# Optimization experiments

Hardware: AMD Instinct MI355X
Metric: run time of the kernel (lower is better)

The kernel has to match this reference:

```python
import jax, jax.numpy as jnp
import numpy as np
import math

N_NODES = 16000
N_EDGES = 256000
F = 64            # channels per irrep (hidden = 64x0e + 64x1o)
Z = 4             # num chemical elements
R = 8             # radial embedding dim
AVG_NN = 16.0
LS = (0, 1, 2)
OFF = {0: 0, 1: 1, 2: 4}
DIM = {0: 1, 1: 3, 2: 5}
SH_DIM = 9
# tensor-product paths (l1, l2, l3), parity-allowed (l1+l2+l3 even), l3 <= 2
PATHS_I0 = ((0, 0, 0), (0, 1, 1), (0, 2, 2))
PATHS_I1 = ((0, 0, 0), (0, 1, 1), (0, 2, 2), (1, 0, 1), (1, 1, 0), (1, 1, 2), (1, 2, 1))
PATHS_P = ((0, 0, 0), (0, 1, 1), (0, 2, 2), (1, 0, 1), (1, 1, 0), (1, 1, 2), (1, 2, 1), (2, 0, 2), (2, 1, 1), (2, 2, 0), (2, 2, 2))


def _cg_complex(l1, l2, l3):
    f = math.factorial
    C = np.zeros((2 * l1 + 1, 2 * l2 + 1, 2 * l3 + 1))
    pre0 = math.sqrt((2 * l3 + 1) * f(l3 + l1 - l2) * f(l3 - l1 + l2) * f(l1 + l2 - l3) / f(l1 + l2 + l3 + 1))
    for m1 in range(-l1, l1 + 1):
        for m2 in range(-l2, l2 + 1):
            m3 = m1 + m2
            if abs(m3) > l3:
                continue
            pre = pre0 * math.sqrt(f(l3 + m3) * f(l3 - m3) * f(l1 - m1) * f(l1 + m1) * f(l2 - m2) * f(l2 + m2))
            s = 0.0
            for k in range(0, l1 + l2 - l3 + 1):
                d = (k, l1 + l2 - l3 - k, l1 - m1 - k, l2 + m2 - k, l3 - l2 + m1 + k, l3 - l1 - m2 + k)
                if min(d) < 0:
                    continue
                den = 1.0
                for x in d:
                    den *= f(x)
                s += (-1) ** k / den
            C[m1 + l1, m2 + l2, m3 + l3] = pre * s
    return C


def _c2r(l):
    # complex -> real spherical-harmonic change of basis (rows: real m, cols: complex m)
    A = np.zeros((2 * l + 1, 2 * l + 1), dtype=complex)
    A[l, l] = 1.0
    s = 1.0 / math.sqrt(2.0)
    for m in range(1, l + 1):
        A[l + m, l + m] = (-1) ** m * s
        A[l + m, l - m] = s
        A[l - m, l + m] = -1j * (-1) ** m * s
        A[l - m, l - m] = 1j * s
    return A


def _real_cg(l1, l2, l3):
    C = np.einsum('ai,bj,ck,ijk->abc', _c2r(l1).conj(), _c2r(l2).conj(), _c2r(l3), _cg_complex(l1, l2, l3))
    Cr = C.real if np.abs(C.real).sum() >= np.abs(C.imag).sum() else C.imag
    n = math.sqrt(float((Cr ** 2).sum()))
    return (Cr / n * math.sqrt(2 * l3 + 1)).astype(np.float32)


CG = {t: jnp.asarray(_real_cg(*t)) for t in PATHS_P}


def setup_inputs() -> dict:
    key = jax.random.key(0)
    ks = iter(jax.random.split(key, 64))

    def nrm(shape, scale):
        return scale * jax.random.normal(next(ks), shape, dtype=jnp.float32)

    def lin(i, o):
        return nrm((i, o), 1.0 / math.sqrt(i))

    inp = {}
    inp['node_feats'] = nrm((N_NODES, F), 1.0)
    inp['node_elem'] = jax.random.randint(next(ks), (N_NODES,), 0, Z, dtype=jnp.int32)
    inp['edge_sh'] = nrm((N_EDGES, SH_DIM), 1.0)
    inp['edge_radial'] = nrm((N_EDGES, R), 1.0)
    inp['senders'] = jax.random.randint(next(ks), (N_EDGES,), 0, N_NODES, dtype=jnp.int32)
    inp['receivers'] = jax.random.randint(next(ks), (N_EDGES,), 0, N_NODES, dtype=jnp.int32)
    # interaction block 0 (node feats are scalars only)
    inp['up0_l0'] = lin(F, F)
    inp['r0_w0'] = lin(R, F); inp['r0_w1'] = lin(F, F); inp['r0_w2'] = lin(F, F)
    inp['r0_wo'] = lin(F, len(PATHS_I0) * F)
    inp['lin0_l0'] = lin(F, F); inp['lin0_l1'] = lin(F, F); inp['lin0_l2'] = lin(F, F)
    inp['sc0_l0'] = nrm((Z, F, F), 1.0 / math.sqrt(F))
    inp['p0_w2'] = nrm((Z, len(PATHS_P), F), 0.1)
    inp['p0_w3'] = nrm((Z, len(PATHS_P), F), 0.1)
    inp['p0_wnu'] = nrm((Z, 3, 2, F), 0.3)
    inp['p0_lin_l0'] = lin(F, F); inp['p0_lin_l1'] = lin(F, F)
    # interaction block 1 (node feats are 64x0e + 64x1o)
    inp['up1_l0'] = lin(F, F); inp['up1_l1'] = lin(F, F)
    inp['r1_w0'] = lin(R, F); inp['r1_w1'] = lin(F, F); inp['r1_w2'] = lin(F, F)
    inp['r1_wo'] = lin(F, len(PATHS_I1) * F)
    inp['lin1_l0'] = lin(2 * F, F); inp['lin1_l1'] = lin(3 * F, F); inp['lin1_l2'] = lin(2 * F, F)
    inp['sc1_l0'] = nrm((Z, F, F), 1.0 / math.sqrt(F))
    inp['sc1_l1'] = nrm((Z, F, F), 1.0 / math.sqrt(F))
    inp['p1_w2'] = nrm((Z, len(PATHS_P), F), 0.1)
    inp['p1_w3'] = nrm((Z, len(PATHS_P), F), 0.1)
    inp['p1_wnu'] = nrm((Z, 3, 2, F), 0.3)
    inp['p1_lin_l0'] = lin(F, F); inp['p1_lin_l1'] = lin(F, F)
    return inp


def _forward(node_feats, node_elem, edge_sh, edge_radial, senders, receivers, P):
    one_hot = jax.nn.one_hot(node_elem, Z, dtype=node_feats.dtype)  # [N, Z]
    sh = {l: edge_sh[:, OFF[l]:OFF[l] + DIM[l]] for l in LS}        # per-l angular blocks
    x = {0: node_feats[:, :, None]}                                 # {l: [N, F, 2l+1]}
    feats_list = []
    for b in range(2):
        paths = PATHS_I0 if b == 0 else PATHS_I1
        scw = {0: P['sc0_l0']} if b == 0 else {0: P['sc1_l0'], 1: P['sc1_l1']}
        # element-dependent skip connection (FullyConnectedTP with one-hot 0e attrs)
        sc = {}
        for l in (0, 1):
            if l in scw:
                sc[l] = jnp.einsum('nki,nz,zkc->nci', x[l], one_hot, scw[l])
            else:
                sc[l] = jnp.zeros((N_NODES, F, DIM[l]), node_feats.dtype)
        # linear_up per irrep
        y = {l: jnp.einsum('nki,kc->nci', x[l], P['up%d_l%d' % (b, l)]) for l in x}
        # radial MLP -> per-edge, per-path, per-channel tp weights
        h = edge_radial
        for W in (P['r%d_w0' % b], P['r%d_w1' % b], P['r%d_w2' % b]):
            h = jax.nn.silu(h @ W)
        w = (h @ P['r%d_wo' % b]).reshape(N_EDGES, len(paths), F)
        # edge tensor product + scatter (message passing)
        by_l3 = {l: [] for l in LS}
        for p, (l1, l2, l3) in enumerate(paths):
            m = jnp.einsum('eki,ej,ijm->ekm', y[l1][senders], sh[l2], CG[(l1, l2, l3)])
            agg = jax.ops.segment_sum(m * w[:, p, :, None], receivers, num_segments=N_NODES) / AVG_NN
            by_l3[l3].append(agg)
        A = {l3: jnp.einsum('npi,pc->nci', jnp.concatenate(v, axis=1), P['lin%d_l%d' % (b, l3)])
             for l3, v in by_l3.items()}
        # equivariant product basis, correlation order 3 (iterated CG with element weights)
        Ts = [A]
        T = A
        for wp in (P['p%d_w2' % b], P['p%d_w3' % b]):
            Tn = {l: jnp.zeros_like(A[l]) for l in LS}
            for p, (l1, l2, l3) in enumerate(PATHS_P):
                c = (one_hot @ wp[:, p, :])[:, :, None]  # [N, F, 1]
                Tn[l3] = Tn[l3] + c * jnp.einsum('nki,nkj,ijm->nkm', T[l1], A[l2], CG[(l1, l2, l3)])
            T = Tn
            Ts.append(Tn)
        wnu = P['p%d_wnu' % b]
        xn = {}
        for Li, L in enumerate((0, 1)):
            B = sum((one_hot @ wnu[:, nu, Li, :])[:, :, None] * Ts[nu][L] for nu in range(3))
            xn[L] = jnp.einsum('nki,kc->nci', B, P['p%d_lin_l%d' % (b, L)]) + sc[L]
        x = xn
        feats_list.append(jnp.concatenate([x[0].reshape(N_NODES, -1), x[1].reshape(N_NODES, -1)], axis=-1))
    return jnp.concatenate(feats_list, axis=-1)  # [N, 2*(F + 3F)] = [N, 512]


def reference(node_feats, node_elem, edge_sh, edge_radial, senders, receivers, up0_l0, r0_w0, r0_w1, r0_w2, r0_wo, lin0_l0, lin0_l1, lin0_l2, sc0_l0, p0_w2, p0_w3, p0_wnu, p0_lin_l0, p0_lin_l1, up1_l0, up1_l1, r1_w0, r1_w1, r1_w2, r1_wo, lin1_l0, lin1_l1, lin1_l2, sc1_l0, sc1_l1, p1_w2, p1_w3, p1_wnu, p1_lin_l0, p1_lin_l1):
    P = dict(locals())
    return _forward(node_feats, node_elem, edge_sh, edge_radial, senders, receivers, P)
```

## Files before the change

kernel.cpp:

```cpp
#include <hip/hip_runtime.h>
#include <hip/hip_bf16.h>
#include <math.h>

#define NNODES 16000
#define NEDGES 256000

typedef float v2f __attribute__((ext_vector_type(2)));
typedef short bf16x8 __attribute__((ext_vector_type(8)));
typedef float f32x4 __attribute__((ext_vector_type(4)));

#define WS_CG   0
#define WS_Y0   512
#define WS_Y1   (WS_Y0 + NNODES*64)
#define WS_SC0  (WS_Y1 + NNODES*192)
#define WS_SC1  (WS_SC0 + NNODES*64)
#define WS_BIG  (WS_SC1 + NNODES*192)
#define WS_AGG  WS_BIG
#define WS_X0N  (WS_BIG + NNODES*9*64)
#define WS_X1N  (WS_X0N + NNODES*64)
#define WS_CSR  (WS_BIG + NNODES*21*64)
#define WS_WPK  (WS_CSR + 310000)
#define WS_WBUF (WS_WPK + 18432)


__device__ __forceinline__ float silu_f(float x) { return x / (1.f + expf(-x)); }

__device__ __forceinline__ void c2r_elem(int l, int r, int c, double& re, double& im) {
  re = 0.0; im = 0.0;
  int mr = r - l, mc = c - l;
  const double s = 0.70710678118654752440;
  if (mr == 0) { if (mc == 0) re = 1.0; return; }
  if (mr > 0) {
    double sg = (mr & 1) ? -1.0 : 1.0;
    if (mc == mr) re = sg * s;
    else if (mc == -mr) re = s;
  } else {
    int m = -mr;
    double sg = (m & 1) ? -1.0 : 1.0;
    if (mc == m) im = -sg * s;
    else if (mc == -m) im = s;
  }
}

__constant__ int CG_L1[11] = {0,0,0,1,1,1,1,2,2,2,2};
__constant__ int CG_L2[11] = {0,1,2,0,1,1,2,0,1,2,2};
__constant__ int CG_L3[11] = {0,1,2,1,0,2,1,2,1,0,2};
__constant__ int CG_OFF[11] = {0,1,10,35,44,53,98,143,168,213,238};
__constant__ double CG_FACT[8] = {1.,1.,2.,6.,24.,120.,720.,5040.};

__launch_bounds__(512)
__global__ void k_cg(float* __restrict__ cg) {
  __shared__ double CCs[11][125];
  __shared__ double trs[11*125];
  __shared__ double tis[11*125];
  __shared__ double scaleL[11];
  __shared__ int useRL[11];
  int tid = threadIdx.x;

  for (int i = tid; i < 11*125; i += 512) CCs[i/125][i%125] = 0.0;
  __syncthreads();

  for (int idx = tid; idx < 11*25; idx += 512) {
    int p = idx / 25, r = idx % 25;
    int i1 = r / 5, i2 = r % 5;
    int l1 = CG_L1[p], l2 = CG_L2[p], l3 = CG_L3[p];
    int d2 = 2*l2+1, d3 = 2*l3+1;
    if (i1 >= 2*l1+1 || i2 >= d2) continue;
    int m1 = i1 - l1, m2 = i2 - l2, m3 = m1 + m2;
    if (m3 < -l3 || m3 > l3) continue;
    double pre0 = sqrt((double)(2*l3+1) * CG_FACT[l3+l1-l2] * CG_FACT[l3-l1+l2]
                       * CG_FACT[l1+l2-l3] / CG_FACT[l1+l2+l3+1]);
    double pre = pre0 * sqrt(CG_FACT[l3+m3]*CG_FACT[l3-m3]*CG_FACT[l1-m1]
                             *CG_FACT[l1+m1]*CG_FACT[l2-m2]*CG_FACT[l2+m2]);
    double ssum = 0.0;
    for (int k = 0; k <= l1 + l2 - l3; k++) {
      int a2 = l1-m1-k, a3 = l2+m2-k, a4 = l3-l2+m1+k, a5 = l3-l1-m2+k;
      if (a2 < 0 || a3 < 0 || a4 < 0 || a5 < 0) continue;
      double den = CG_FACT[k]*CG_FACT[l1+l2-l3-k]*CG_FACT[a2]*CG_FACT[a3]*CG_FACT[a4]*CG_FACT[a5];
      ssum += ((k & 1) ? -1.0 : 1.0) / den;
    }
    CCs[p][(i1*d2 + i2)*d3 + (m3 + l3)] = pre * ssum;
  }
  __syncthreads();

  for (int idx = tid; idx < 11*125; idx += 512) {
    int p = idx / 125, r = idx % 125;
    int a = r / 25, b = (r / 5) % 5, c = r % 5;
    int l1 = CG_L1[p], l2 = CG_L2[p], l3 = CG_L3[p];
    int d1 = 2*l1+1, d2 = 2*l2+1, d3 = 2*l3+1;
    if (a >= d1 || b >= d2 || c >= d3) continue;
    double tr = 0.0, ti = 0.0;
    for (int i = 0; i < d1; i++) for (int j = 0; j < d2; j++) {
      double a1r, a1i, a2r, a2i;
      c2r_elem(l1, a, i, a1r, a1i); a1i = -a1i;
      c2r_elem(l2, b, j, a2r, a2i); a2i = -a2i;
      double zr = a1r*a2r - a1i*a2i, zi = a1r*a2i + a1i*a2r;
      for (int k = 0; k < d3; k++) {
        double cc = CCs[p][(i*d2 + j)*d3 + k];
        if (cc == 0.0) continue;
        double a3r, a3i;
        c2r_elem(l3, c, k, a3r, a3i);
        tr += (zr*a3r - zi*a3i) * cc;
        ti += (zr*a3i + zi*a3r) * cc;
      }
    }
    trs[idx] = tr; tis[idx] = ti;
  }
  __syncthreads();

  if (tid < 11) {
    int p = tid;
    int l1 = CG_L1[p], l2 = CG_L2[p], l3 = CG_L3[p];
    int d1 = 2*l1+1, d2 = 2*l2+1, d3 = 2*l3+1;
    double sr = 0.0, si = 0.0;
    for (int a = 0; a < d1; a++) for (int b = 0; b < d2; b++) for (int c = 0; c < d3; c++) {
      int idx = p*125 + a*25 + b*5 + c;
      sr += fabs(trs[idx]); si += fabs(tis[idx]);
    }
    int useR = (sr >= si);
    double nrm = 0.0;
    for (int a = 0; a < d1; a++) for (int b = 0; b < d2; b++) for (int c = 0; c < d3; c++) {
      int idx = p*125 + a*25 + b*5 + c;
      double v = useR ? trs[idx] : tis[idx];
      nrm += v * v;
    }
    scaleL[p] = sqrt((double)(2*l3+1)) / sqrt(nrm);
    useRL[p] = useR;
  }
  __syncthreads();

  for (int idx = tid; idx < 11*125; idx += 512) {
    int p = idx / 125, r = idx % 125;
    int a = r / 25, b = (r / 5) % 5, c = r % 5;
    int l1 = CG_L1[p], l2 = CG_L2[p], l3 = CG_L3[p];
    int d1 = 2*l1+1, d2 = 2*l2+1, d3 = 2*l3+1;
    if (a >= d1 || b >= d2 || c >= d3) continue;
    double v = useRL[p] ? trs[idx] : tis[idx];
    cg[CG_OFF[p] + (a*d2 + b)*d3 + c] = (float)(v * scaleL[p]);
  }
}

__global__ void k_hist(const int* __restrict__ recv, int* __restrict__ counts) {
  int e = blockIdx.x * 256 + threadIdx.x;
  if (e < NEDGES) atomicAdd(&counts[recv[e]], 1);
}

__launch_bounds__(256)
__global__ void k_scan(const int* __restrict__ counts, int* __restrict__ off, int* __restrict__ cursor) {
  __shared__ int part[256];
  __shared__ int base[257];
  int t = threadIdx.x;
  const int CH = (NNODES + 255) / 256;
  int s = 0;
  for (int i = 0; i < CH; i++) { int n = t*CH + i; if (n < NNODES) s += counts[n]; }
  part[t] = s;
  __syncthreads();
  if (t == 0) { int acc = 0; for (int i = 0; i < 256; i++) { base[i] = acc; acc += part[i]; } base[256] = acc; }
  __syncthreads();
  int run = base[t];
  for (int i = 0; i < CH; i++) {
    int n = t*CH + i;
    if (n < NNODES) { int cn = counts[n]; off[n] = run; cursor[n] = run; run += cn; }
  }
  if (t == 255) off[NNODES] = base[256];
}

__global__ void k_bucket(const int* __restrict__ recv, int* __restrict__ cursor, int* __restrict__ eidx) {
  int e = blockIdx.x * 256 + threadIdx.x;
  if (e < NEDGES) { int p = atomicAdd(&cursor[recv[e]], 1); eidx[p] = e; }
}

template<int B>
__global__ void k_wprep(const float* __restrict__ w1, const float* __restrict__ w2,
                        const float* __restrict__ wo, __hip_bfloat16* __restrict__ wpk) {
  constexpr int NP = B ? 7 : 3;
  constexpr int NWO = 2 * NP*4 * 64 * 8;
  int idx = blockIdx.x * 256 + threadIdx.x;
  const float* w; int Nout, NOC, local, base;
  if (idx < 4096)            { w = w1; Nout = 64;    NOC = 4;    local = idx;        base = 0; }
  else if (idx < 8192)       { w = w2; Nout = 64;    NOC = 4;    local = idx - 4096; base = 4096; }
  else if (idx < 8192 + NWO) { w = wo; Nout = NP*64; NOC = NP*4; local = idx - 8192; base = 8192; }
  else return;
  int i = local & 7, lane = (local >> 3) & 63, rest = local >> 9;
  int oc = rest % NOC, ks = rest / NOC;
  int k = ks*32 + ((lane >> 4) * 8) + i;
  int col = oc*16 + (lane & 15);
  wpk[base + local] = __float2bfloat16(w[k*Nout + col]);
}

template<int D1, int D2, int D3, int BASE, int ROWS>
__device__ __forceinline__ void tp_acc(const float (&yv)[D1], const float* shv, float wsc,
                                       const float* cgs, int offc, float (&acc)[ROWS]) {
  float m[D3];
#pragma unroll
  for (int mm = 0; mm < D3; mm++) m[mm] = 0.f;
#pragma unroll
  for (int i = 0; i < D1; i++)
#pragma unroll
    for (int j = 0; j < D2; j++) {
      float t = yv[i] * shv[j];
#pragma unroll
      for (int mm = 0; mm < D3; mm++) m[mm] += t * cgs[offc + (i*D2 + j)*D3 + mm];
    }
  float s = wsc * (1.f / 16.f);
#pragma unroll
  for (int mm = 0; mm < D3; mm++) acc[BASE + mm] += s * m[mm];
}

template<int ROWS>
__device__ __forceinline__ void flush_acc(float (&acc)[ROWS], float* __restrict__ Agg,
                                          int rn, int lane) {
  float* aggn = Agg + (size_t)rn * (ROWS*64);
#pragma unroll
  for (int r = 0; r < ROWS; r++) {
    unsafeAtomicAdd(&aggn[r*64 + lane], acc[r]);
    acc[r] = 0.f;
  }
}

template<int D1, int D2, int D3>
__device__ __forceinline__ void pb_path(float cp, const float (&T)[D1], const float (&A)[D2],
                                        float (&NN)[D3], const float* cgs, int offc) {
#pragma unroll
  for (int i = 0; i < D1; i++)
#pragma unroll
    for (int j = 0; j < D2; j++) {
      float t = cp * T[i] * A[j];
#pragma unroll
      for (int mm = 0; mm < D3; mm++) NN[mm] += t * cgs[offc + (i*D2 + j)*D3 + mm];
    }
}

template<int B>
__launch_bounds__(256)
__global__ void k_node_pre(const float* __restrict__ x0, const float* __restrict__ x1,
                           const int* __restrict__ elem,
                           const float* __restrict__ upl0, const float* __restrict__ upl1,
                           const float* __restrict__ scw0, const float* __restrict__ scw1,
                           float* __restrict__ y0, float* __restrict__ y1,
                           float* __restrict__ sc0, float* __restrict__ sc1) {
  __shared__ float xs[4][4][64];
  int wid = threadIdx.x >> 6, lane = threadIdx.x & 63;
  int n = blockIdx.x * 4 + wid;
  xs[wid][0][lane] = x0[n*64 + lane];
  if (B) {
#pragma unroll
    for (int i = 0; i < 3; i++) xs[wid][1 + i][lane] = x1[(n*3 + i)*64 + lane];
  }
  __syncthreads();
  int z = elem[n];
  float a0 = 0.f, s0 = 0.f;
  float a1[3] = {0.f,0.f,0.f}, s1[3] = {0.f,0.f,0.f};
  for (int k = 0; k < 64; k++) {
    float xv = xs[wid][0][k];
    a0 += xv * upl0[k*64 + lane];
    s0 += xv * scw0[(z*64 + k)*64 + lane];
    if (B) {
      float uv = upl1[k*64 + lane];
      float sv = scw1[(z*64 + k)*64 + lane];
#pragma unroll
      for (int i = 0; i < 3; i++) {
        float xv1 = xs[wid][1 + i][k];
        a1[i] += xv1 * uv;
        s1[i] += xv1 * sv;
      }
    }
  }
  y0[n*64 + lane] = a0;
  sc0[n*64 + lane] = s0;
  if (B) {
#pragma unroll
    for (int i = 0; i < 3; i++) {
      y1[(n*3 + i)*64 + lane] = a1[i];
      sc1[(n*3 + i)*64 + lane] = s1[i];
    }
  }
}

template<int B>
__launch_bounds__(256)
__global__ void k_mlp(const float* __restrict__ er, const int* __restrict__ eidx,
                      const float* __restrict__ w0, const __hip_bfloat16* __restrict__ wpk,
                      __hip_bfloat16* __restrict__ wbuf, int ebase) {
  constexpr int NP = B ? 7 : 3;
  constexpr int NOC = NP * 4;
  __shared__ __align__(16) __hip_bfloat16 hsb[4][2][16][72];
  int wid = threadIdx.x >> 6, lane = threadIdx.x & 63;
  int g = blockIdx.x * 4 + wid;
  int base = ebase + g * 16;
  int col16 = lane & 15, kg = lane >> 4;

#pragma unroll 1
  for (int j = 0; j < 16; j++) {
    int e = __builtin_amdgcn_readfirstlane(eidx[base + j]);
    float a = 0.f;
#pragma unroll
    for (int r = 0; r < 8; r++) a += er[e*8 + r] * w0[r*64 + lane];
    hsb[wid][0][j][lane] = __float2bfloat16(silu_f(a));
  }

#pragma unroll
  for (int L = 0; L < 2; L++) {
    const __hip_bfloat16* wp = wpk + L * 4096;
    bf16x8 A0 = *(const bf16x8*)&hsb[wid][L][col16][kg*8];
    bf16x8 A1 = *(const bf16x8*)&hsb[wid][L][col16][32 + kg*8];
    f32x4 acc[4];
#pragma unroll
    for (int oc = 0; oc < 4; oc++) acc[oc] = (f32x4){0.f,0.f,0.f,0.f};
#pragma unroll
    for (int ks = 0; ks < 2; ks++) {
      bf16x8 A = ks ? A1 : A0;
#pragma unroll
      for (int oc = 0; oc < 4; oc++) {
        bf16x8 Bf = *(const bf16x8*)&wp[((ks*4 + oc)*64 + lane)*8];
        acc[oc] = __builtin_amdgcn_mfma_f32_16x16x32_bf16(A, Bf, acc[oc], 0, 0, 0);
      }
    }
#pragma unroll
    for (int oc = 0; oc < 4; oc++)
#pragma unroll
      for (int i = 0; i < 4; i++)
        hsb[wid][1 - L][kg*4 + i][oc*16 + col16] = __float2bfloat16(silu_f(acc[oc][i]));
  }

  {
    bf16x8 A0 = *(const bf16x8*)&hsb[wid][0][col16][kg*8];
    bf16x8 A1 = *(const bf16x8*)&hsb[wid][0][col16][32 + kg*8];
    const __hip_bfloat16* wp = wpk + 8192;
#pragma unroll 1
    for (int oc = 0; oc < NOC; oc++) {
      f32x4 acc = (f32x4){0.f,0.f,0.f,0.f};
      bf16x8 B0 = *(const bf16x8*)&wp[((0*NOC + oc)*64 + lane)*8];
      bf16x8 B1 = *(const bf16x8*)&wp[((1*NOC + oc)*64 + lane)*8];
      acc = __builtin_amdgcn_mfma_f32_16x16x32_bf16(A0, B0, acc, 0, 0, 0);
      acc = __builtin_amdgcn_mfma_f32_16x16x32_bf16(A1, B1, acc, 0, 0, 0);
      int p = oc >> 2, chan = (oc & 3)*16 + col16;
#pragma unroll
      for (int i = 0; i < 4; i++) {
        int edge = kg*4 + i;
        wbuf[((size_t)(g*16 + edge) * NP + p)*64 + chan] = __float2bfloat16(acc[i]);
      }
    }
  }
}

template<int B>
__launch_bounds__(256)
__global__ void k_tp(const float* __restrict__ esh,
                     const int* __restrict__ senders, const int* __restrict__ receivers,
                     const int* __restrict__ eidx,
                     const float* __restrict__ y0, const float* __restrict__ y1,
                     const __hip_bfloat16* __restrict__ wbuf, const float* __restrict__ cg,
                     float* __restrict__ Agg, int ebase) {
  constexpr int NP = B ? 7 : 3;
  constexpr int ROWS = B ? 21 : 9;
  constexpr int EPW = 16;
  __shared__ float cgs[363];
  int wid = threadIdx.x >> 6, lane = threadIdx.x & 63;
  for (int i = threadIdx.x; i < 363; i += 256) cgs[i] = cg[i];
  __syncthreads();

  int g = blockIdx.x * 4 + wid;
  int base = ebase + g * EPW;

  float acc[ROWS];
#pragma unroll
  for (int r = 0; r < ROWS; r++) acc[r] = 0.f;
  int rprev = -1;
#pragma unroll 1
  for (int j = 0; j < EPW; j++) {
    int e = __builtin_amdgcn_readfirstlane(eidx[base + j]);
    int r = __builtin_amdgcn_readfirstlane(receivers[e]);
    if (j > 0 && r != rprev) flush_acc<ROWS>(acc, Agg, rprev, lane);
    rprev = r;
    int sn = senders[e];
    const __hip_bfloat16* wj = wbuf + ((size_t)(g*EPW + j)) * NP * 64 + lane;
    float w[NP];
#pragma unroll
    for (int p = 0; p < NP; p++) w[p] = __bfloat162float(wj[p*64]);
    float y0a[1] = { y0[sn*64 + lane] };
    float sh[9];
#pragma unroll
    for (int q = 0; q < 9; q++) sh[q] = esh[e*9 + q];
    if constexpr (B == 0) {
      tp_acc<1,1,1,0>(y0a, sh + 0, w[0], cgs, 0,  acc);
      tp_acc<1,3,3,1>(y0a, sh + 1, w[1], cgs, 1,  acc);
      tp_acc<1,5,5,4>(y0a, sh + 4, w[2], cgs, 10, acc);
    } else {
      tp_acc<1,1,1,0> (y0a, sh + 0, w[0], cgs, 0,  acc);
      tp_acc<1,3,3,2> (y0a, sh + 1, w[1], cgs, 1,  acc);
      tp_acc<1,5,5,11>(y0a, sh + 4, w[2], cgs, 10, acc);
      float y1a[3];
#pragma unroll
      for (int i = 0; i < 3; i++) y1a[i] = y1[(sn*3 + i)*64 + lane];
      tp_acc<3,1,3,5> (y1a, sh + 0, w[3], cgs, 35, acc);
      tp_acc<3,3,1,1> (y1a, sh + 1, w[4], cgs, 44, acc);
      tp_acc<3,3,5,16>(y1a, sh + 1, w[5], cgs, 53, acc);
      tp_acc<3,5,3,8> (y1a, sh + 4, w[6], cgs, 98, acc);
    }
  }
  flush_acc<ROWS>(acc, Agg, rprev, lane);
}

template<int B>
__launch_bounds__(256)
__global__ void k_lin(float* __restrict__ Agg,
                      const float* __restrict__ lin0, const float* __restrict__ lin1,
                      const float* __restrict__ lin2, int npb) {
  constexpr int P0 = B ? 2 : 1, P1 = B ? 3 : 1, P2 = B ? 2 : 1;
  constexpr int ROWS = P0 + 3*P1 + 5*P2;
  constexpr int BASE1 = P0, BASE2 = P0 + 3*P1;
  constexpr int PMAX = (P1 > P2) ? (P1 > P0 ? P1 : P0) : (P2 > P0 ? P2 : P0);
  constexpr int SROWS = (3*P1 > 5*P2) ? (3*P1 > P0 ? 3*P1 : P0) : (5*P2 > P0 ? 5*P2 : P0);
  __shared__ float wlds[PMAX*64*64];
  __shared__ float st[4][SROWS][64];
  int wid = threadIdx.x >> 6, lane = threadIdx.x & 63;
  int n0 = blockIdx.x * npb;
  int nend = n0 + npb; if (nend > NNODES) nend = NNODES;

  for (int i = threadIdx.x; i < P0*64*64; i += 256) wlds[i] = lin0[i];
  __syncthreads();
  for (int n = n0 + wid; n < nend; n += 4) {
    float* an = Agg + (size_t)n * (ROWS*64);
#pragma unroll
    for (int P = 0; P < P0; P++) st[wid][P][lane] = an[P*64 + lane];
    float a = 0.f;
    for (int k = 0; k < 64; k++) {
#pragma unroll
      for (int P = 0; P < P0; P++) a += st[wid][P][k] * wlds[(P*64 + k)*64 + lane];
    }
    an[0*64 + lane] = a;
  }
  __syncthreads();

  for (int i = threadIdx.x; i < P1*64*64; i += 256) wlds[i] = lin1[i];
  __syncthreads();
  for (int n = n0 + wid; n < nend; n += 4) {
    float* an = Agg + (size_t)n * (ROWS*64);
#pragma unroll
    for (int r = 0; r < 3*P1; r++) st[wid][r][lane] = an[(BASE1 + r)*64 + lane];
    float A1[3];
#pragma unroll
    for (int i = 0; i < 3; i++) {
      float a = 0.f;
      for (int k = 0; k < 64; k++) {
#pragma unroll
        for (int P = 0; P < P1; P++) a += st[wid][P*3 + i][k] * wlds[(P*64 + k)*64 + lane];
      }
      A1[i] = a;
    }
#pragma unroll
    for (int i = 0; i < 3; i++) an[(1 + i)*64 + lane] = A1[i];
  }
  __syncthreads();

  for (int i = threadIdx.x; i < P2*64*64; i += 256) wlds[i] = lin2[i];
  __syncthreads();
  for (int n = n0 + wid; n < nend; n += 4) {
    float* an = Agg + (size_t)n * (ROWS*64);
#pragma unroll
    for (int r = 0; r < 5*P2; r++) st[wid][r][lane] = an[(BASE2 + r)*64 + lane];
    float A2[5];
#pragma unroll
    for (int i = 0; i < 5; i++) {
      float a = 0.f;
      for (int k = 0; k < 64; k++) {
#pragma unroll
        for (int P = 0; P < P2; P++) a += st[wid][P*5 + i][k] * wlds[(P*64 + k)*64 + lane];
      }
      A2[i] = a;
    }
#pragma unroll
    for (int i = 0; i < 5; i++) an[(4 + i)*64 + lane] = A2[i];
  }
}

template<int B>
__launch_bounds__(256)
__global__ void k_pbout(const float* __restrict__ Agg, const int* __restrict__ elem,
                        const float* __restrict__ w2p, const float* __restrict__ w3p,
                        const float* __restrict__ wnu, const float* __restrict__ cg,
                        const float* __restrict__ plin0, const float* __restrict__ plin1,
                        const float* __restrict__ sc0, const float* __restrict__ sc1,
                        float* __restrict__ x0n, float* __restrict__ x1n,
                        float* __restrict__ out, int obase, int npb) {
  constexpr int ROWS = B ? 21 : 9;
  __shared__ float cgs[363];
  __shared__ float w2s[4*11*64];
  __shared__ float w3s[4*11*64];
  __shared__ float wns[4*3*2*64];
  __shared__ float p0s[64*64];
  __shared__ float p1s[64*64];
  __shared__ float Bs[4][4][64];
  int wid = threadIdx.x >> 6, lane = threadIdx.x & 63;
  for (int i = threadIdx.x; i < 363; i += 256) cgs[i] = cg[i];
  for (int i = threadIdx.x; i < 4*11*64; i += 256) { w2s[i] = w2p[i]; w3s[i] = w3p[i]; }
  for (int i = threadIdx.x; i < 4*3*2*64; i += 256) wns[i] = wnu[i];
  for (int i = threadIdx.x; i < 64*64; i += 256) { p0s[i] = plin0[i]; p1s[i] = plin1[i]; }
  __syncthreads();

  int n0 = blockIdx.x * npb;
  int nend = n0 + npb; if (nend > NNODES) nend = NNODES;
  for (int n = n0 + wid; n < nend; n += 4) {
    int z = elem[n];
    const float* an = Agg + (size_t)n * (ROWS*64);
    float A0[1] = { an[0*64 + lane] };
    float A1[3], A2[5];
#pragma unroll
    for (int i = 0; i < 3; i++) A1[i] = an[(1 + i)*64 + lane];
#pragma unroll
    for (int i = 0; i < 5; i++) A2[i] = an[(4 + i)*64 + lane];

    float T0[1] = {A0[0]};
    float T1[3], T2[5];
#pragma unroll
    for (int i = 0; i < 3; i++) T1[i] = A1[i];
#pragma unroll
    for (int i = 0; i < 5; i++) T2[i] = A2[i];
    float s10 = 0.f, s11[3] = {0.f,0.f,0.f}, s20 = 0.f, s21[3] = {0.f,0.f,0.f};
#pragma unroll
    for (int it = 0; it < 2; it++) {
      const float* wp = it ? w3s : w2s;
      float c[11];
#pragma unroll
      for (int p = 0; p < 11; p++) c[p] = wp[(z*11 + p)*64 + lane];
      float n0v[1] = {0.f}, n1v[3] = {0.f,0.f,0.f}, n2v[5] = {0.f,0.f,0.f,0.f,0.f};
      pb_path<1,1,1>(c[0],  T0, A0, n0v, cgs, 0);
      pb_path<1,3,3>(c[1],  T0, A1, n1v, cgs, 1);
      pb_path<1,5,5>(c[2],  T0, A2, n2v, cgs, 10);
      pb_path<3,1,3>(c[3],  T1, A0, n1v, cgs, 35);
      pb_path<3,3,1>(c[4],  T1, A1, n0v, cgs, 44);
      pb_path<3,3,5>(c[5],  T1, A1, n2v, cgs, 53);
      pb_path<3,5,3>(c[6],  T1, A2, n1v, cgs, 98);
      pb_path<5,1,5>(c[7],  T2, A0, n2v, cgs, 143);
      pb_path<5,3,3>(c[8],  T2, A1, n1v, cgs, 168);
      pb_path<5,5,1>(c[9],  T2, A2, n0v, cgs, 213);
      pb_path<5,5,5>(c[10], T2, A2, n2v, cgs, 238);
      T0[0] = n0v[0];
#pragma unroll
      for (int i = 0; i < 3; i++) T1[i] = n1v[i];
#pragma unroll
      for (int i = 0; i < 5; i++) T2[i] = n2v[i];
      if (it == 0) {
        s10 = n0v[0];
#pragma unroll
        for (int i = 0; i < 3; i++) s11[i] = n1v[i];
      } else {
        s20 = n0v[0];
#pragma unroll
        for (int i = 0; i < 3; i++) s21[i] = n1v[i];
      }
    }

    float c00 = wns[((z*3 + 0)*2 + 0)*64 + lane];
    float c10 = wns[((z*3 + 1)*2 + 0)*64 + lane];
    float c20 = wns[((z*3 + 2)*2 + 0)*64 + lane];
    float c01 = wns[((z*3 + 0)*2 + 1)*64 + lane];
    float c11 = wns[((z*3 + 1)*2 + 1)*64 + lane];
    float c21 = wns[((z*3 + 2)*2 + 1)*64 + lane];
    Bs[wid][0][lane] = c00*A0[0] + c10*s10 + c20*s20;
#pragma unroll
    for (int i = 0; i < 3; i++)
      Bs[wid][1 + i][lane] = c01*A1[i] + c11*s11[i] + c21*s21[i];

    float x0v = 0.f, x1v[3] = {0.f,0.f,0.f};
    for (int k = 0; k < 64; k++) {
      float p0v = p0s[k*64 + lane];
      float p1v = p1s[k*64 + lane];
      x0v += Bs[wid][0][k] * p0v;
#pragma unroll
      for (int i = 0; i < 3; i++) x1v[i] += Bs[wid][1 + i][k] * p1v;
    }
    x0v += sc0[n*64 + lane];
    if (B) {
#pragma unroll
      for (int i = 0; i < 3; i++) x1v[i] += sc1[(n*3 + i)*64 + lane];
    }
    if (B == 0) {
      x0n[n*64 + lane] = x0v;
#pragma unroll
      for (int i = 0; i < 3; i++) x1n[(n*3 + i)*64 + lane] = x1v[i];
    }
    out[(size_t)n*512 + obase + lane] = x0v;
#pragma unroll
    for (int i = 0; i < 3; i++)
      out[(size_t)n*512 + obase + 64 + lane*3 + i] = x1v[i];
  }
}

extern "C" void kernel_launch(void* const* d_in, const int* in_sizes, int n_in,
                              void* d_out, int out_size, void* d_ws, size_t ws_size,
                              hipStream_t stream) {
  const float* node_feats  = (const float*)d_in[0];
  const int*   node_elem   = (const int*)  d_in[1];
  const float* edge_sh     = (const float*)d_in[2];
  const float* edge_radial = (const float*)d_in[3];
  const int*   senders     = (const int*)  d_in[4];
  const int*   receivers   = (const int*)  d_in[5];
  const float* up0_l0   = (const float*)d_in[6];
  const float* r0_w0    = (const float*)d_in[7];
  const float* r0_w1    = (const float*)d_in[8];
  const float* r0_w2    = (const float*)d_in[9];
  const float* r0_wo    = (const float*)d_in[10];
  const float* lin0_l0  = (const float*)d_in[11];
  const float* lin0_l1  = (const float*)d_in[12];
  const float* lin0_l2  = (const float*)d_in[13];
  const float* sc0_l0   = (const float*)d_in[14];
  const float* p0_w2    = (const float*)d_in[15];
  const float* p0_w3    = (const float*)d_in[16];
  const float* p0_wnu   = (const float*)d_in[17];
  const float* p0_lin_l0= (const float*)d_in[18];
  const float* p0_lin_l1= (const float*)d_in[19];
  const float* up1_l0   = (const float*)d_in[20];
  const float* up1_l1   = (const float*)d_in[21];
  const float* r1_w0    = (const float*)d_in[22];
  const float* r1_w1    = (const float*)d_in[23];
  const float* r1_w2    = (const float*)d_in[24];
  const float* r1_wo    = (const float*)d_in[25];
  const float* lin1_l0  = (const float*)d_in[26];
  const float* lin1_l1  = (const float*)d_in[27];
  const float* lin1_l2  = (const float*)d_in[28];
  const float* sc1_l0   = (const float*)d_in[29];
  const float* sc1_l1   = (const float*)d_in[30];
  const float* p1_w2    = (const float*)d_in[31];
  const float* p1_w3    = (const float*)d_in[32];
  const float* p1_wnu   = (const float*)d_in[33];
  const float* p1_lin_l0= (const float*)d_in[34];
  const float* p1_lin_l1= (const float*)d_in[35];

  float* ws  = (float*)d_ws;
  float* cg  = ws + WS_CG;
  float* y0  = ws + WS_Y0;
  float* y1  = ws + WS_Y1;
  float* sc0 = ws + WS_SC0;
  float* sc1 = ws + WS_SC1;
  float* x0n = ws + WS_X0N;
  float* x1n = ws + WS_X1N;
  float* Agg = ws + WS_AGG;
  int* counts = (int*)(ws + WS_CSR);
  int* off    = counts + NNODES;
  int* cursor = off + NNODES + 1;
  int* eidx   = cursor + NNODES;
  __hip_bfloat16* wpk  = (__hip_bfloat16*)(ws + WS_WPK);
  __hip_bfloat16* wbuf = (__hip_bfloat16*)(ws + WS_WBUF);
  float* out = (float*)d_out;

  size_t cap_bytes = (ws_size > (size_t)WS_WBUF*4) ? ws_size - (size_t)WS_WBUF*4 : 0;
  int chunk = 131072;
  if (cap_bytes < (size_t)chunk * 7 * 64 * 2) {
    chunk = (int)((cap_bytes / (7*64*2)) & ~(size_t)63);
    if (chunk < 64) chunk = 64;
  }
  const int NPB = 32;
  const int NODE_BLOCKS = (NNODES + NPB - 1) / NPB;

  k_cg<<<1, 512, 0, stream>>>(cg);

  hipMemsetAsync(counts, 0, NNODES * sizeof(int), stream);
  k_hist<<<(NEDGES + 255) / 256, 256, 0, stream>>>(receivers, counts);
  k_scan<<<1, 256, 0, stream>>>(counts, off, cursor);
  k_bucket<<<(NEDGES + 255) / 256, 256, 0, stream>>>(receivers, cursor, eidx);

  k_node_pre<0><<<NNODES/4, 256, 0, stream>>>(node_feats, nullptr, node_elem,
                                              up0_l0, nullptr, sc0_l0, nullptr,
                                              y0, y1, sc0, sc1);
  hipMemsetAsync(Agg, 0, (size_t)NNODES * 9 * 64 * sizeof(float), stream);
  k_wprep<0><<<(8192 + 2*3*4*512 + 255)/256, 256, 0, stream>>>(r0_w1, r0_w2, r0_wo, wpk);
  for (int e0 = 0; e0 < NEDGES; e0 += chunk) {
    int ce = (NEDGES - e0 < chunk) ? (NEDGES - e0) : chunk;
    k_mlp<0><<<ce/64, 256, 0, stream>>>(edge_radial, eidx, r0_w0, wpk, wbuf, e0);
    k_tp<0><<<ce/64, 256, 0, stream>>>(edge_sh, senders, receivers, eidx, y0, y1, wbuf, cg, Agg, e0);
  }
  k_lin<0><<<NODE_BLOCKS, 256, 0, stream>>>(Agg, lin0_l0, lin0_l1, lin0_l2, NPB);
  k_pbout<0><<<NODE_BLOCKS, 256, 0, stream>>>(Agg, node_elem, p0_w2, p0_w3, p0_wnu, cg,
                                              p0_lin_l0, p0_lin_l1, sc0, sc1,
                                              x0n, x1n, out, 0, NPB);

  k_node_pre<1><<<NNODES/4, 256, 0, stream>>>(x0n, x1n, node_elem,
                                              up1_l0, up1_l1, sc1_l0, sc1_l1,
                                              y0, y1, sc0, sc1);
  hipMemsetAsync(Agg, 0, (size_t)NNODES * 21 * 64 * sizeof(float), stream);
  k_wprep<1><<<(8192 + 2*7*4*512 + 255)/256, 256, 0, stream>>>(r1_w1, r1_w2, r1_wo, wpk);
  for (int e0 = 0; e0 < NEDGES; e0 += chunk) {
    int ce = (NEDGES - e0 < chunk) ? (NEDGES - e0) : chunk;
    k_mlp<1><<<ce/64, 256, 0, stream>>>(edge_radial, eidx, r1_w0, wpk, wbuf, e0);
    k_tp<1><<<ce/64, 256, 0, stream>>>(edge_sh, senders, receivers, eidx, y0, y1, wbuf, cg, Agg, e0);
  }
  k_lin<1><<<NODE_BLOCKS, 256, 0, stream>>>(Agg, lin1_l0, lin1_l1, lin1_l2, NPB);
  k_pbout<1><<<NODE_BLOCKS, 256, 0, stream>>>(Agg, node_elem, p1_w2, p1_w3, p1_wnu, cg,
                                              p1_lin_l0, p1_lin_l1, sc0, sc1,
                                              x0n, x1n, out, 256, NPB);
}
```

Measured before the change: 1.014 ms.

## Rewrite per-node linear layers with bf16 MFMA and prepacked weights

Replaces the scalar fp32 LDS-based k_lin with a kernel that runs each linear phase as 16x16x32 bf16 MFMA tiles over 16 nodes per block. A new k_linprep kernel packs the linear weights into bf16 fragment order ahead of time, and activations are converted to bf16 as they are loaded. The aim is to cut the FMA-bound cost of the per-node channel mixing, at the price of bf16 precision on both activations and weights.

```diff
diff --git a/kernel.cpp b/kernel.cpp
--- a/kernel.cpp
+++ b/kernel.cpp
@@ -20,10 +20,22 @@
 #define WS_X1N  (WS_X0N + NNODES*64)
 #define WS_CSR  (WS_BIG + NNODES*21*64)
 #define WS_WPK  (WS_CSR + 310000)
-#define WS_WBUF (WS_WPK + 18432)
+#define WS_WLPK (WS_WPK + 18432)
+#define WS_WBUF (WS_WLPK + 14336)
 
 
 __device__ __forceinline__ float silu_f(float x) { return x / (1.f + expf(-x)); }
+__device__ __forceinline__ short f2bs(float x) {
+  __hip_bfloat16 h = __float2bfloat16(x);
+  return *reinterpret_cast<short*>(&h);
+}
+__device__ __forceinline__ bf16x8 cvt8(const float* p) {
+  float4 a = *(const float4*)p, b = *(const float4*)(p + 4);
+  bf16x8 r;
+  r[0]=f2bs(a.x); r[1]=f2bs(a.y); r[2]=f2bs(a.z); r[3]=f2bs(a.w);
+  r[4]=f2bs(b.x); r[5]=f2bs(b.y); r[6]=f2bs(b.z); r[7]=f2bs(b.w);
+  return r;
+}
 
 __device__ __forceinline__ void c2r_elem(int l, int r, int c, double& re, double& im) {
   re = 0.0; im = 0.0;
@@ -188,6 +200,24 @@
   wpk[base + local] = __float2bfloat16(w[k*Nout + col]);
 }
 
+template<int B>
+__global__ void k_linprep(const float* __restrict__ lin0, const float* __restrict__ lin1,
+                          const float* __restrict__ lin2, __hip_bfloat16* __restrict__ wlpk) {
+  constexpr int KS0 = (B?2:1)*2, KS1 = (B?3:1)*2, KS2 = (B?2:1)*2;
+  constexpr int N0 = KS0*2048, N1 = KS1*2048, N2 = KS2*2048;
+  int idx = blockIdx.x * 256 + threadIdx.x;
+  const float* w; int local, base;
+  if (idx < N0)           { w = lin0; local = idx;          base = 0; }
+  else if (idx < N0+N1)   { w = lin1; local = idx - N0;     base = N0; }
+  else if (idx < N0+N1+N2){ w = lin2; local = idx - N0-N1;  base = N0+N1; }
+  else return;
+  int i = local & 7, lane = (local >> 3) & 63, rest = local >> 9;
+  int oc = rest & 3, ks = rest >> 2;
+  int k = ks*32 + ((lane >> 4) * 8) + i;
+  int col = oc*16 + (lane & 15);
+  wlpk[base + local] = __float2bfloat16(w[k*64 + col]);
+}
+
 template<int D1, int D2, int D3, int BASE, int ROWS>
 __device__ __forceinline__ void tp_acc(const float (&yv)[D1], const float* shv, float wsc,
                                        const float* cgs, int offc, float (&acc)[ROWS]) {
@@ -402,76 +432,57 @@
   flush_acc<ROWS>(acc, Agg, rprev, lane);
 }
 
+template<int D, int KS>
+__device__ __forceinline__ void lin_phase(const float* __restrict__ anA, int rowsx64_unused,
+                                          const __hip_bfloat16* __restrict__ wp,
+                                          int oc, int lane, int inbase, int stride64,
+                                          f32x4 (&acc)[D]) {
+#pragma unroll
+  for (int i = 0; i < D; i++) {
+    f32x4 a = (f32x4){0.f,0.f,0.f,0.f};
+#pragma unroll
+    for (int ks = 0; ks < KS; ks++) {
+      int kglob = ks*32 + ((lane >> 4) * 8);
+      int P = kglob >> 6, ch = kglob & 63;
+      bf16x8 A = cvt8(anA + (inbase + P*stride64 + i)*64 + ch);
+      bf16x8 Bf = *(const bf16x8*)&wp[((ks*4 + oc)*64 + lane)*8];
+      a = __builtin_amdgcn_mfma_f32_16x16x32_bf16(A, Bf, a, 0, 0, 0);
+    }
+    acc[i] = a;
+  }
+}
+
 template<int B>
 __launch_bounds__(256)
-__global__ void k_lin(float* __restrict__ Agg,
-                      const float* __restrict__ lin0, const float* __restrict__ lin1,
-                      const float* __restrict__ lin2, int npb) {
+__global__ void k_lin(float* __restrict__ Agg, const __hip_bfloat16* __restrict__ wlpk) {
   constexpr int P0 = B ? 2 : 1, P1 = B ? 3 : 1, P2 = B ? 2 : 1;
   constexpr int ROWS = P0 + 3*P1 + 5*P2;
   constexpr int BASE1 = P0, BASE2 = P0 + 3*P1;
-  constexpr int PMAX = (P1 > P2) ? (P1 > P0 ? P1 : P0) : (P2 > P0 ? P2 : P0);
-  constexpr int SROWS = (3*P1 > 5*P2) ? (3*P1 > P0 ? 3*P1 : P0) : (5*P2 > P0 ? 5*P2 : P0);
-  __shared__ float wlds[PMAX*64*64];
-  __shared__ float st[4][SROWS][64];
+  constexpr int KS0 = P0*2, KS1 = P1*2, KS2 = P2*2;
+  constexpr int OFF1 = KS0*2048, OFF2 = OFF1 + KS1*2048;
   int wid = threadIdx.x >> 6, lane = threadIdx.x & 63;
-  int n0 = blockIdx.x * npb;
-  int nend = n0 + npb; if (nend > NNODES) nend = NNODES;
-
-  for (int i = threadIdx.x; i < P0*64*64; i += 256) wlds[i] = lin0[i];
-  __syncthreads();
-  for (int n = n0 + wid; n < nend; n += 4) {
-    float* an = Agg + (size_t)n * (ROWS*64);
-#pragma unroll
-    for (int P = 0; P < P0; P++) st[wid][P][lane] = an[P*64 + lane];
-    float a = 0.f;
-    for (int k = 0; k < 64; k++) {
-#pragma unroll
-      for (int P = 0; P < P0; P++) a += st[wid][P][k] * wlds[(P*64 + k)*64 + lane];
-    }
-    an[0*64 + lane] = a;
-  }
-  __syncthreads();
-
-  for (int i = threadIdx.x; i < P1*64*64; i += 256) wlds[i] = lin1[i];
-  __syncthreads();
-  for (int n = n0 + wid; n < nend; n += 4) {
-    float* an = Agg + (size_t)n * (ROWS*64);
-#pragma unroll
-    for (int r = 0; r < 3*P1; r++) st[wid][r][lane] = an[(BASE1 + r)*64 + lane];
-    float A1[3];
-#pragma unroll
-    for (int i = 0; i < 3; i++) {
-      float a = 0.f;
-      for (int k = 0; k < 64; k++) {
-#pragma unroll
-        for (int P = 0; P < P1; P++) a += st[wid][P*3 + i][k] * wlds[(P*64 + k)*64 + lane];
-      }
-      A1[i] = a;
-    }
-#pragma unroll
-    for (int i = 0; i < 3; i++) an[(1 + i)*64 + lane] = A1[i];
-  }
-  __syncthreads();
-
-  for (int i = threadIdx.x; i < P2*64*64; i += 256) wlds[i] = lin2[i];
-  __syncthreads();
-  for (int n = n0 + wid; n < nend; n += 4) {
-    float* an = Agg + (size_t)n * (ROWS*64);
-#pragma unroll
-    for (int r = 0; r < 5*P2; r++) st[wid][r][lane] = an[(BASE2 + r)*64 + lane];
-    float A2[5];
-#pragma unroll
-    for (int i = 0; i < 5; i++) {
-      float a = 0.f;
-      for (int k = 0; k < 64; k++) {
-#pragma unroll
-        for (int P = 0; P < P2; P++) a += st[wid][P*5 + i][k] * wlds[(P*64 + k)*64 + lane];
-      }
-      A2[i] = a;
-    }
-#pragma unroll
-    for (int i = 0; i < 5; i++) an[(4 + i)*64 + lane] = A2[i];
+  int oc = wid;
+  int n0 = blockIdx.x * 16;
+  int m = lane & 15;
+  const float* anA = Agg + (size_t)(n0 + m) * (ROWS*64);
+
+  f32x4 a0[1], a1[3], a2[5];
+  lin_phase<1, KS0>(anA, 0, wlpk,        oc, lane, 0,     1, a0);
+  lin_phase<3, KS1>(anA, 0, wlpk + OFF1, oc, lane, BASE1, 3, a1);
+  lin_phase<5, KS2>(anA, 0, wlpk + OFF2, oc, lane, BASE2, 5, a2);
+
+  __syncthreads();
+
+  int col = oc*16 + (lane & 15);
+  int kg = lane >> 4;
+#pragma unroll
+  for (int r = 0; r < 4; r++) {
+    float* an = Agg + (size_t)(n0 + kg*4 + r) * (ROWS*64);
+    an[0*64 + col] = a0[0][r];
+#pragma unroll
+    for (int i = 0; i < 3; i++) an[(1 + i)*64 + col] = a1[i][r];
+#pragma unroll
+    for (int i = 0; i < 5; i++) an[(4 + i)*64 + col] = a2[i][r];
   }
 }
 
@@ -642,6 +653,7 @@
   int* cursor = off + NNODES + 1;
   int* eidx   = cursor + NNODES;
   __hip_bfloat16* wpk  = (__hip_bfloat16*)(ws + WS_WPK);
+  __hip_bfloat16* wlpk = (__hip_bfloat16*)(ws + WS_WLPK);
   __hip_bfloat16* wbuf = (__hip_bfloat16*)(ws + WS_WBUF);
   float* out = (float*)d_out;
 
@@ -666,12 +678,13 @@
                                               y0, y1, sc0, sc1);
   hipMemsetAsync(Agg, 0, (size_t)NNODES * 9 * 64 * sizeof(float), stream);
   k_wprep<0><<<(8192 + 2*3*4*512 + 255)/256, 256, 0, stream>>>(r0_w1, r0_w2, r0_wo, wpk);
+  k_linprep<0><<<(6*2048 + 255)/256, 256, 0, stream>>>(lin0_l0, lin0_l1, lin0_l2, wlpk);
   for (int e0 = 0; e0 < NEDGES; e0 += chunk) {
     int ce = (NEDGES - e0 < chunk) ? (NEDGES - e0) : chunk;
     k_mlp<0><<<ce/64, 256, 0, stream>>>(edge_radial, eidx, r0_w0, wpk, wbuf, e0);
     k_tp<0><<<ce/64, 256, 0, stream>>>(edge_sh, senders, receivers, eidx, y0, y1, wbuf, cg, Agg, e0);
   }
-  k_lin<0><<<NODE_BLOCKS, 256, 0, stream>>>(Agg, lin0_l0, lin0_l1, lin0_l2, NPB);
+  k_lin<0><<<NNODES/16, 256, 0, stream>>>(Agg, wlpk);
   k_pbout<0><<<NODE_BLOCKS, 256, 0, stream>>>(Agg, node_elem, p0_w2, p0_w3, p0_wnu, cg,
                                               p0_lin_l0, p0_lin_l1, sc0, sc1,
                                               x0n, x1n, out, 0, NPB);
@@ -681,12 +694,13 @@
                                               y0, y1, sc0, sc1);
   hipMemsetAsync(Agg, 0, (size_t)NNODES * 21 * 64 * sizeof(float), stream);
   k_wprep<1><<<(8192 + 2*7*4*512 + 255)/256, 256, 0, stream>>>(r1_w1, r1_w2, r1_wo, wpk);
+  k_linprep<1><<<(14*2048 + 255)/256, 256, 0, stream>>>(lin1_l0, lin1_l1, lin1_l2, wlpk);
   for (int e0 = 0; e0 < NEDGES; e0 += chunk) {
     int ce = (NEDGES - e0 < chunk) ? (NEDGES - e0) : chunk;
     k_mlp<1><<<ce/64, 256, 0, stream>>>(edge_radial, eidx, r1_w0, wpk, wbuf, e0);
     k_tp<1><<<ce/64, 256, 0, stream>>>(edge_sh, senders, receivers, eidx, y0, y1, wbuf, cg, Agg, e0);
   }
-  k_lin<1><<<NODE_BLOCKS, 256, 0, stream>>>(Agg, lin1_l0, lin1_l1, lin1_l2, NPB);
+  k_lin<1><<<NNODES/16, 256, 0, stream>>>(Agg, wlpk);
   k_pbout<1><<<NODE_BLOCKS, 256, 0, stream>>>(Agg, node_elem, p1_w2, p1_w3, p1_wnu, cg,
                                               p1_lin_l0, p1_lin_l1, sc0, sc1,
                                               x0n, x1n, out, 256, NPB);
```

Result: faster. 914.6 us (-9.8%).
